# Kernel optimization log

Hardware: AMD Instinct MI355X
Metric: run time of the kernel (lower is better)

The kernel has to match this reference:

```python
import jax, jax.numpy as jnp
import numpy as np

HEADS, OUT_CH = 8, 32  # GATConv(128, 256//8, heads=8) -> concat width 256
NEG_SLOPE = 0.2


def setup_inputs() -> dict:
    key = jax.random.key(0)
    ks = jax.random.split(key, 12)
    N, E, F_IN = 50000, 500000, 128
    H, C = HEADS, OUT_CH
    HID = H * C            # 256
    x = jax.random.normal(ks[0], (N, F_IN), dtype=jnp.float32)
    edge_index = jax.random.randint(ks[1], (2, E), 0, N, dtype=jnp.int64)
    s = 1.0 / np.sqrt(F_IN)
    W_gat = jax.random.normal(ks[2], (F_IN, H * C), dtype=jnp.float32) * s
    att_src = jax.random.normal(ks[3], (H, C), dtype=jnp.float32) * (1.0 / np.sqrt(C))
    att_dst = jax.random.normal(ks[4], (H, C), dtype=jnp.float32) * (1.0 / np.sqrt(C))
    b_gat = jnp.zeros((HID,), dtype=jnp.float32)
    W1 = jax.random.normal(ks[5], (HID, HID // 2), dtype=jnp.float32) * (1.0 / np.sqrt(HID))
    b1 = jnp.zeros((HID // 2,), dtype=jnp.float32)
    W2 = jax.random.normal(ks[6], (HID // 2, 6), dtype=jnp.float32) * (1.0 / np.sqrt(HID // 2))
    b2 = jnp.zeros((6,), dtype=jnp.float32)
    return {"x": x, "edge_index": edge_index, "W_gat": W_gat, "att_src": att_src,
            "att_dst": att_dst, "b_gat": b_gat, "W1": W1, "b1": b1, "W2": W2, "b2": b2}


def _gat_forward(x, edge_index, W_gat, att_src, att_dst, b_gat):
    N = x.shape[0]
    H, C = HEADS, OUT_CH
    # add self loops (PyG GATConv default)
    loop = jnp.arange(N, dtype=edge_index.dtype)
    src = jnp.concatenate([edge_index[0], loop])
    dst = jnp.concatenate([edge_index[1], loop])
    # per-node transform: [N, H, C]
    xh = (x @ W_gat).reshape(N, H, C)
    a_src = jnp.einsum('nhc,hc->nh', xh, att_src)  # [N, H]
    a_dst = jnp.einsum('nhc,hc->nh', xh, att_dst)  # [N, H]
    alpha = a_src[src] + a_dst[dst]                # [Etot, H]
    alpha = jnp.where(alpha >= 0, alpha, NEG_SLOPE * alpha)  # leaky relu
    # segment softmax over destination nodes
    m = jax.ops.segment_max(alpha, dst, num_segments=N)     # [N, H]
    m = jax.lax.stop_gradient(m)
    ex = jnp.exp(alpha - m[dst])
    denom = jax.ops.segment_sum(ex, dst, num_segments=N)    # [N, H]
    coef = ex / denom[dst]                                   # [Etot, H]
    # weighted scatter-add aggregation
    msgs = xh[src] * coef[:, :, None]                        # [Etot, H, C]
    out = jax.ops.segment_sum(msgs, dst, num_segments=N)     # [N, H, C]
    return out.reshape(N, H * C) + b_gat


def reference(x, edge_index, W_gat, att_src, att_dst, b_gat, W1, b1, W2, b2):
    h = _gat_forward(x, edge_index, W_gat, att_src, att_dst, b_gat)
    h = jax.nn.elu(h)
    g = jnp.mean(h, axis=0, keepdims=True)   # [1, 256] mean pool
    g = jax.nn.relu(g @ W1 + b1)
    return g @ W2 + b2                        # [1, 6] logits
```

## Files before the change

kernel.cpp:

```cpp
#include <hip/hip_runtime.h>
#include <hip/hip_fp8.h>
#include <math.h>

#define F_IN 128
#define HID 256
#define NH 8
#define CAP 40

typedef _Float16 h16;
typedef __attribute__((ext_vector_type(8))) _Float16 half8;
typedef __attribute__((ext_vector_type(4))) float f32x4;

__device__ inline unsigned char f32_to_fp8(float v) {
#if __has_builtin(__builtin_amdgcn_cvt_pk_fp8_f32)
    return (unsigned char)(__builtin_amdgcn_cvt_pk_fp8_f32(v, v, 0, false) & 0xff);
#else
    __hip_fp8_e4m3 t(v);
    return (unsigned char)t.__x;
#endif
}

__device__ inline void fp8x4_to_f32(int w, float* out) {
#if __has_builtin(__builtin_amdgcn_cvt_pk_f32_fp8)
    auto lo = __builtin_amdgcn_cvt_pk_f32_fp8(w, false);
    auto hi = __builtin_amdgcn_cvt_pk_f32_fp8(w, true);
    out[0] = lo[0]; out[1] = lo[1]; out[2] = hi[0]; out[3] = hi[1];
#else
    #pragma unroll
    for (int k = 0; k < 4; ++k) {
        __hip_fp8_e4m3 t;
        t.__x = (unsigned char)((w >> (8 * k)) & 0xff);
        out[k] = (float)t;
    }
#endif
}

__global__ void k_prep(const float* __restrict__ Wg, h16* __restrict__ Wt_sw,
                       int* cnt, float* g2, int n) {
    int i = blockIdx.x * 256 + threadIdx.x;
    if (i < n) cnt[i] = 0;
    if (i < 256 * HID) g2[i] = 0.f;
    if (i < 4096) {
        int fid = i;
        int lane16 = fid & 15;
        int quad = (fid >> 4) & 3;
        int ks = (fid >> 6) & 3;
        int ct = fid >> 8;
        int col = ct * 16 + lane16;
        int k0 = ks * 32 + quad * 8;
        half8 v;
        #pragma unroll
        for (int j = 0; j < 8; ++j) v[j] = (h16)Wg[(size_t)(k0 + j) * HID + col];
        *(half8*)(Wt_sw + (size_t)fid * 8) = v;
    }
}

__global__ __launch_bounds__(512) void k_gemmsc(const float* __restrict__ x,
                                                const h16* __restrict__ Wt_sw,
                                                const float* __restrict__ att_s,
                                                const float* __restrict__ att_d,
                                                const int* __restrict__ srcp,
                                                const int* __restrict__ dstp,
                                                unsigned char* __restrict__ xh8,
                                                float* __restrict__ a_src,
                                                float* __restrict__ a_dst,
                                                int* cnt, unsigned short* __restrict__ bin,
                                                int n, int e, int ntiles) {
    __shared__ h16 wlds[32768];
    int t = threadIdx.x;
    {
        const int4* wsrc = (const int4*)Wt_sw;
        int4* wdst = (int4*)wlds;
        #pragma unroll
        for (int i = 0; i < 8; ++i) wdst[i * 512 + t] = wsrc[i * 512 + t];
    }
    __syncthreads();
    int w = t >> 6, l = t & 63;
    int lane16 = l & 15, quad = l >> 4;
    const h16* wl = wlds + (size_t)l * 8;

    auto do_gemm = [&]() {
        for (int tile = blockIdx.x * 8 + w; tile < ntiles; tile += gridDim.x * 8) {
            int row0 = tile * 16;
            int rA = row0 + lane16;
            if (rA >= n) rA = n - 1;
            const float* xrow = x + (size_t)rA * F_IN + quad * 8;
            half8 afr[4];
            #pragma unroll
            for (int ks = 0; ks < 4; ++ks) {
                float4 v0 = *(const float4*)(xrow + ks * 32);
                float4 v1 = *(const float4*)(xrow + ks * 32 + 4);
                half8 a;
                a[0] = (h16)v0.x; a[1] = (h16)v0.y; a[2] = (h16)v0.z; a[3] = (h16)v0.w;
                a[4] = (h16)v1.x; a[5] = (h16)v1.y; a[6] = (h16)v1.z; a[7] = (h16)v1.w;
                afr[ks] = a;
            }
            f32x4 acc[16];
            #pragma unroll
            for (int ct = 0; ct < 16; ++ct) acc[ct] = (f32x4){0.f, 0.f, 0.f, 0.f};
            #pragma unroll
            for (int ct = 0; ct < 16; ++ct) {
                #pragma unroll
                for (int ks = 0; ks < 4; ++ks) {
                    half8 b = *(const half8*)(wl + (ct * 4 + ks) * 512);
                    acc[ct] = __builtin_amdgcn_mfma_f32_16x16x32_f16(afr[ks], b, acc[ct], 0, 0, 0);
                }
            }
            if (row0 + 16 <= n) {
                #pragma unroll
                for (int ct = 0; ct < 16; ++ct) {
                    int col = ct * 16 + lane16;
                    #pragma unroll
                    for (int r = 0; r < 4; ++r)
                        xh8[(size_t)(row0 + quad * 4 + r) * HID + col] = f32_to_fp8(acc[ct][r]);
                }
            } else {
                #pragma unroll
                for (int ct = 0; ct < 16; ++ct) {
                    int col = ct * 16 + lane16;
                    #pragma unroll
                    for (int r = 0; r < 4; ++r) {
                        int row = row0 + quad * 4 + r;
                        if (row < n) xh8[(size_t)row * HID + col] = f32_to_fp8(acc[ct][r]);
                    }
                }
            }
            #pragma unroll
            for (int h = 0; h < 8; ++h) {
                float ps[4] = {0.f, 0.f, 0.f, 0.f};
                float pd[4] = {0.f, 0.f, 0.f, 0.f};
                #pragma unroll
                for (int cc = 0; cc < 2; ++cc) {
                    int ct = h * 2 + cc;
                    float as_ = att_s[ct * 16 + lane16];
                    float ad_ = att_d[ct * 16 + lane16];
                    #pragma unroll
                    for (int r = 0; r < 4; ++r) {
                        ps[r] += acc[ct][r] * as_;
                        pd[r] += acc[ct][r] * ad_;
                    }
                }
                #pragma unroll
                for (int m = 1; m < 16; m <<= 1) {
                    #pragma unroll
                    for (int r = 0; r < 4; ++r) {
                        ps[r] += __shfl_xor(ps[r], m, 64);
                        pd[r] += __shfl_xor(pd[r], m, 64);
                    }
                }
                if (lane16 == 0) {
                    #pragma unroll
                    for (int r = 0; r < 4; ++r) {
                        int row = row0 + quad * 4 + r;
                        if (row < n) {
                            a_src[row * NH + h] = ps[r];
                            a_dst[row * NH + h] = pd[r];
                        }
                    }
                }
            }
        }
    };
    auto do_scatter = [&]() {
        for (int i = blockIdx.x * 512 + t; i < e; i += gridDim.x * 512) {
            int d = dstp[i];
            int pos = atomicAdd(&cnt[d], 1);
            if (pos < CAP) bin[(size_t)d * CAP + pos] = (unsigned short)srcp[i];
        }
    };
    if (blockIdx.x & 1) { do_scatter(); do_gemm(); }
    else                { do_gemm(); do_scatter(); }
}

__global__ __launch_bounds__(256) void k_agg(const unsigned char* __restrict__ xh8,
                                             const float* __restrict__ a_src,
                                             const float* __restrict__ a_dst,
                                             const int* __restrict__ cnt,
                                             const unsigned short* __restrict__ bin,
                                             const float* __restrict__ b_gat,
                                             float* __restrict__ g2, int n) {
    __shared__ float wpart[4][260];
    int t = threadIdx.x;
    int slot = t >> 4;
    int cl = t & 15;
    int c0 = cl * 16;
    int h = cl >> 1;
    int nn = blockIdx.x * 16 + slot;
    bool alive = nn < n;
    int nnc = alive ? nn : (n - 1);

    float ad = a_dst[nnc * NH + h];
    int deg = cnt[nnc];
    if (deg > CAP) deg = CAP;

    float al = a_src[nnc * NH + h] + ad;
    al = al > 0.f ? al : 0.2f * al;
    float ex = __expf(al);
    float den = ex;
    float acc[16];
    {
        int4 v = *(const int4*)(xh8 + (size_t)nnc * HID + c0);
        float f[16];
        fp8x4_to_f32(v.x, f); fp8x4_to_f32(v.y, f + 4);
        fp8x4_to_f32(v.z, f + 8); fp8x4_to_f32(v.w, f + 12);
        #pragma unroll
        for (int i = 0; i < 16; ++i) acc[i] = ex * f[i];
    }
    const unsigned short* brow = bin + (size_t)nnc * CAP;
    int j = 0;
    for (; j + 4 <= deg; j += 4) {
        ushort4 ss = *(const ushort4*)(brow + j);
        int s0 = ss.x, s1 = ss.y, s2 = ss.z, s3 = ss.w;
        float aa[4];
        aa[0] = a_src[s0 * NH + h];
        aa[1] = a_src[s1 * NH + h];
        aa[2] = a_src[s2 * NH + h];
        aa[3] = a_src[s3 * NH + h];
        int4 v0 = *(const int4*)(xh8 + (size_t)s0 * HID + c0);
        int4 v1 = *(const int4*)(xh8 + (size_t)s1 * HID + c0);
        int4 v2 = *(const int4*)(xh8 + (size_t)s2 * HID + c0);
        int4 v3 = *(const int4*)(xh8 + (size_t)s3 * HID + c0);
        float e4[4];
        #pragma unroll
        for (int q = 0; q < 4; ++q) {
            float a2 = aa[q] + ad;
            a2 = a2 > 0.f ? a2 : 0.2f * a2;
            e4[q] = __expf(a2);
            den += e4[q];
        }
        float f[16];
        fp8x4_to_f32(v0.x, f); fp8x4_to_f32(v0.y, f + 4);
        fp8x4_to_f32(v0.z, f + 8); fp8x4_to_f32(v0.w, f + 12);
        #pragma unroll
        for (int i = 0; i < 16; ++i) acc[i] += e4[0] * f[i];
        fp8x4_to_f32(v1.x, f); fp8x4_to_f32(v1.y, f + 4);
        fp8x4_to_f32(v1.z, f + 8); fp8x4_to_f32(v1.w, f + 12);
        #pragma unroll
        for (int i = 0; i < 16; ++i) acc[i] += e4[1] * f[i];
        fp8x4_to_f32(v2.x, f); fp8x4_to_f32(v2.y, f + 4);
        fp8x4_to_f32(v2.z, f + 8); fp8x4_to_f32(v2.w, f + 12);
        #pragma unroll
        for (int i = 0; i < 16; ++i) acc[i] += e4[2] * f[i];
        fp8x4_to_f32(v3.x, f); fp8x4_to_f32(v3.y, f + 4);
        fp8x4_to_f32(v3.z, f + 8); fp8x4_to_f32(v3.w, f + 12);
        #pragma unroll
        for (int i = 0; i < 16; ++i) acc[i] += e4[3] * f[i];
    }
    for (; j < deg; ++j) {
        int s = brow[j];
        float a2 = a_src[s * NH + h] + ad;
        a2 = a2 > 0.f ? a2 : 0.2f * a2;
        float e2 = __expf(a2);
        den += e2;
        int4 v = *(const int4*)(xh8 + (size_t)s * HID + c0);
        float f[16];
        fp8x4_to_f32(v.x, f); fp8x4_to_f32(v.y, f + 4);
        fp8x4_to_f32(v.z, f + 8); fp8x4_to_f32(v.w, f + 12);
        #pragma unroll
        for (int i = 0; i < 16; ++i) acc[i] += e2 * f[i];
    }
    float inv = 1.f / den;
    float val[16];
    #pragma unroll
    for (int q = 0; q < 4; ++q) {
        float4 bv = *(const float4*)(b_gat + c0 + q * 4);
        val[q * 4 + 0] = acc[q * 4 + 0] * inv + bv.x;
        val[q * 4 + 1] = acc[q * 4 + 1] * inv + bv.y;
        val[q * 4 + 2] = acc[q * 4 + 2] * inv + bv.z;
        val[q * 4 + 3] = acc[q * 4 + 3] * inv + bv.w;
    }
    #pragma unroll
    for (int i = 0; i < 16; ++i) {
        float v = val[i];
        v = v > 0.f ? v : expm1f(v);
        val[i] = alive ? v : 0.f;
    }
    #pragma unroll
    for (int i = 0; i < 16; ++i) {
        val[i] += __shfl_xor(val[i], 16, 64);
        val[i] += __shfl_xor(val[i], 32, 64);
    }
    int w = t >> 6, lw = t & 63;
    if (lw < 16) {
        #pragma unroll
        for (int q = 0; q < 4; ++q)
            *(f32x4*)(&wpart[w][c0 + q * 4]) =
                (f32x4){val[q * 4], val[q * 4 + 1], val[q * 4 + 2], val[q * 4 + 3]};
    }
    __syncthreads();
    float s = wpart[0][t] + wpart[1][t] + wpart[2][t] + wpart[3][t];
    atomicAdd(&g2[(blockIdx.x & 255) * HID + t], s);
}

__global__ __launch_bounds__(256) void k_mlp(const float* __restrict__ g2,
                                             const float* __restrict__ W1,
                                             const float* __restrict__ b1,
                                             const float* __restrict__ W2,
                                             const float* __restrict__ b2,
                                             float* __restrict__ out, int n) {
    __shared__ float gm[HID];
    __shared__ float h1p[2][128];
    __shared__ float h1[128];
    int t = threadIdx.x;
    float s = 0.f;
    for (int b = 0; b < 256; ++b) s += g2[b * HID + t];
    gm[t] = s / (float)n;
    __syncthreads();
    int o = t & 127, hf = t >> 7;
    float a = 0.f;
    #pragma unroll 4
    for (int k = hf * 128; k < hf * 128 + 128; ++k) a += gm[k] * W1[k * 128 + o];
    h1p[hf][o] = a;
    __syncthreads();
    if (t < 128) {
        float v = h1p[0][t] + h1p[1][t] + b1[t];
        h1[t] = v > 0.f ? v : 0.f;
    }
    __syncthreads();
    if (t < 6) {
        float a2 = b2[t];
        for (int k = 0; k < 128; ++k) a2 += h1[k] * W2[k * 6 + t];
        out[t] = a2;
    }
}

extern "C" void kernel_launch(void* const* d_in, const int* in_sizes, int n_in,
                              void* d_out, int out_size, void* d_ws, size_t ws_size,
                              hipStream_t stream) {
    const float* x     = (const float*)d_in[0];
    const int*   ei    = (const int*)d_in[1];
    const float* Wg    = (const float*)d_in[2];
    const float* att_s = (const float*)d_in[3];
    const float* att_d = (const float*)d_in[4];
    const float* b_gat = (const float*)d_in[5];
    const float* W1    = (const float*)d_in[6];
    const float* b1    = (const float*)d_in[7];
    const float* W2    = (const float*)d_in[8];
    const float* b2    = (const float*)d_in[9];

    int N = in_sizes[0] / F_IN;
    int E = in_sizes[1] / 2;
    const int* srcp = ei;
    const int* dstp = ei + E;
    int nblk = (N + 15) / 16;
    int ntiles = (N + 15) / 16;

    char* ws = (char*)d_ws;
    size_t off = 0;
    auto alloc = [&](size_t bytes) {
        size_t o = off;
        off += (bytes + 255) & ~(size_t)255;
        return o;
    };
    unsigned char* xh8 = (unsigned char*)(ws + alloc((size_t)N * HID));
    h16*   Wt      = (h16*)(ws + alloc((size_t)F_IN * HID * 2));
    float* asr     = (float*)(ws + alloc((size_t)N * NH * 4));
    float* ads     = (float*)(ws + alloc((size_t)N * NH * 4));
    int*   cnt     = (int*)(ws + alloc((size_t)N * 4));
    unsigned short* bin = (unsigned short*)(ws + alloc((size_t)N * CAP * 2));
    float* g2      = (float*)(ws + alloc((size_t)256 * HID * 4));

    k_prep<<<(N + 255) / 256, 256, 0, stream>>>(Wg, Wt, cnt, g2, N);
    k_gemmsc<<<512, 512, 0, stream>>>(x, Wt, att_s, att_d, srcp, dstp,
                                      xh8, asr, ads, cnt, bin, N, E, ntiles);
    k_agg<<<nblk, 256, 0, stream>>>(xh8, asr, ads, cnt, bin, b_gat, g2, N);
    k_mlp<<<1, 256, 0, stream>>>(g2, W1, b1, W2, b2, (float*)d_out, N);
}
```

Before: 179.6 us.

## Fold attention vectors into GEMM weights and split output columns across block pairs

Precomputes W_gat·att_src and W_gat·att_dst per head as an extra 16-column fp16 weight tile, so a_src/a_dst come from one extra MFMA instead of per-head dot products and shuffle reductions. The GEMM kernel now launches twice as many blocks, with each block pair splitting the 256 output columns in half. This halves LDS use and accumulator registers, which should raise occupancy. The cost is that each x row tile is loaded and converted by both blocks, and the fp16 rounding of the folded weights changes attention-logit precision.

```diff
diff --git a/kernel.cpp b/kernel.cpp
--- a/kernel.cpp
+++ b/kernel.cpp
@@ -35,7 +35,10 @@
 #endif
 }
 
-__global__ void k_prep(const float* __restrict__ Wg, h16* __restrict__ Wt_sw,
+__global__ void k_prep(const float* __restrict__ Wg,
+                       const float* __restrict__ att_s,
+                       const float* __restrict__ att_d,
+                       h16* __restrict__ Wt_sw,
                        int* cnt, float* g2, int n) {
     int i = blockIdx.x * 256 + threadIdx.x;
     if (i < n) cnt[i] = 0;
@@ -53,12 +56,28 @@
         for (int j = 0; j < 8; ++j) v[j] = (h16)Wg[(size_t)(k0 + j) * HID + col];
         *(half8*)(Wt_sw + (size_t)fid * 8) = v;
     }
+    if (i < 256) {
+        int lane16 = i & 15;
+        int quad = (i >> 4) & 3;
+        int ks = i >> 6;
+        int h = lane16 & 7;
+        const float* att = (lane16 < 8) ? att_s : att_d;
+        int k0 = ks * 32 + quad * 8;
+        half8 v;
+        #pragma unroll
+        for (int j = 0; j < 8; ++j) {
+            float s = 0.f;
+            #pragma unroll 8
+            for (int c = 0; c < 32; ++c)
+                s += Wg[(size_t)(k0 + j) * HID + h * 32 + c] * att[h * 32 + c];
+            v[j] = (h16)s;
+        }
+        *(half8*)(Wt_sw + 32768 + (size_t)i * 8) = v;
+    }
 }
 
 __global__ __launch_bounds__(512) void k_gemmsc(const float* __restrict__ x,
                                                 const h16* __restrict__ Wt_sw,
-                                                const float* __restrict__ att_s,
-                                                const float* __restrict__ att_d,
                                                 const int* __restrict__ srcp,
                                                 const int* __restrict__ dstp,
                                                 unsigned char* __restrict__ xh8,
@@ -66,21 +85,29 @@
                                                 float* __restrict__ a_dst,
                                                 int* cnt, unsigned short* __restrict__ bin,
                                                 int n, int e, int ntiles) {
-    __shared__ h16 wlds[32768];
+    __shared__ h16 wlds[18432];
     int t = threadIdx.x;
+    int halfsel = blockIdx.x & 1;
     {
         const int4* wsrc = (const int4*)Wt_sw;
         int4* wdst = (int4*)wlds;
-        #pragma unroll
-        for (int i = 0; i < 8; ++i) wdst[i * 512 + t] = wsrc[i * 512 + t];
+        if (halfsel == 0) {
+            #pragma unroll
+            for (int i = 0; i < 4; ++i) wdst[i * 512 + t] = wsrc[i * 512 + t];
+            if (t < 256) wdst[2048 + t] = wsrc[4096 + t];
+        } else {
+            #pragma unroll
+            for (int i = 0; i < 4; ++i) wdst[i * 512 + t] = wsrc[2048 + i * 512 + t];
+        }
     }
     __syncthreads();
     int w = t >> 6, l = t & 63;
     int lane16 = l & 15, quad = l >> 4;
     const h16* wl = wlds + (size_t)l * 8;
+    int coff = halfsel * 8;
 
     auto do_gemm = [&]() {
-        for (int tile = blockIdx.x * 8 + w; tile < ntiles; tile += gridDim.x * 8) {
+        for (int tile = (blockIdx.x >> 1) * 8 + w; tile < ntiles; tile += (gridDim.x >> 1) * 8) {
             int row0 = tile * 16;
             int rA = row0 + lane16;
             if (rA >= n) rA = n - 1;
@@ -95,11 +122,11 @@
                 a[4] = (h16)v1.x; a[5] = (h16)v1.y; a[6] = (h16)v1.z; a[7] = (h16)v1.w;
                 afr[ks] = a;
             }
-            f32x4 acc[16];
-            #pragma unroll
-            for (int ct = 0; ct < 16; ++ct) acc[ct] = (f32x4){0.f, 0.f, 0.f, 0.f};
-            #pragma unroll
-            for (int ct = 0; ct < 16; ++ct) {
+            f32x4 acc[8];
+            #pragma unroll
+            for (int ct = 0; ct < 8; ++ct) acc[ct] = (f32x4){0.f, 0.f, 0.f, 0.f};
+            #pragma unroll
+            for (int ct = 0; ct < 8; ++ct) {
                 #pragma unroll
                 for (int ks = 0; ks < 4; ++ks) {
                     half8 b = *(const half8*)(wl + (ct * 4 + ks) * 512);
@@ -108,16 +135,16 @@
             }
             if (row0 + 16 <= n) {
                 #pragma unroll
-                for (int ct = 0; ct < 16; ++ct) {
-                    int col = ct * 16 + lane16;
+                for (int ct = 0; ct < 8; ++ct) {
+                    int col = (ct + coff) * 16 + lane16;
                     #pragma unroll
                     for (int r = 0; r < 4; ++r)
                         xh8[(size_t)(row0 + quad * 4 + r) * HID + col] = f32_to_fp8(acc[ct][r]);
                 }
             } else {
                 #pragma unroll
-                for (int ct = 0; ct < 16; ++ct) {
-                    int col = ct * 16 + lane16;
+                for (int ct = 0; ct < 8; ++ct) {
+                    int col = (ct + coff) * 16 + lane16;
                     #pragma unroll
                     for (int r = 0; r < 4; ++r) {
                         int row = row0 + quad * 4 + r;
@@ -125,37 +152,19 @@
                     }
                 }
             }
-            #pragma unroll
-            for (int h = 0; h < 8; ++h) {
-                float ps[4] = {0.f, 0.f, 0.f, 0.f};
-                float pd[4] = {0.f, 0.f, 0.f, 0.f};
-                #pragma unroll
-                for (int cc = 0; cc < 2; ++cc) {
-                    int ct = h * 2 + cc;
-                    float as_ = att_s[ct * 16 + lane16];
-                    float ad_ = att_d[ct * 16 + lane16];
-                    #pragma unroll
-                    for (int r = 0; r < 4; ++r) {
-                        ps[r] += acc[ct][r] * as_;
-                        pd[r] += acc[ct][r] * ad_;
-                    }
-                }
-                #pragma unroll
-                for (int m = 1; m < 16; m <<= 1) {
-                    #pragma unroll
-                    for (int r = 0; r < 4; ++r) {
-                        ps[r] += __shfl_xor(ps[r], m, 64);
-                        pd[r] += __shfl_xor(pd[r], m, 64);
-                    }
-                }
-                if (lane16 == 0) {
-                    #pragma unroll
-                    for (int r = 0; r < 4; ++r) {
-                        int row = row0 + quad * 4 + r;
-                        if (row < n) {
-                            a_src[row * NH + h] = ps[r];
-                            a_dst[row * NH + h] = pd[r];
-                        }
+            if (halfsel == 0) {
+                f32x4 acca = (f32x4){0.f, 0.f, 0.f, 0.f};
+                #pragma unroll
+                for (int ks = 0; ks < 4; ++ks) {
+                    half8 b = *(const half8*)(wl + (32 + ks) * 512);
+                    acca = __builtin_amdgcn_mfma_f32_16x16x32_f16(afr[ks], b, acca, 0, 0, 0);
+                }
+                #pragma unroll
+                for (int r = 0; r < 4; ++r) {
+                    int row = row0 + quad * 4 + r;
+                    if (row < n) {
+                        if (lane16 < 8) a_src[row * NH + lane16] = acca[r];
+                        else            a_dst[row * NH + lane16 - 8] = acca[r];
                     }
                 }
             }
@@ -168,8 +177,8 @@
             if (pos < CAP) bin[(size_t)d * CAP + pos] = (unsigned short)srcp[i];
         }
     };
-    if (blockIdx.x & 1) { do_scatter(); do_gemm(); }
-    else                { do_gemm(); do_scatter(); }
+    if (halfsel) { do_scatter(); do_gemm(); }
+    else         { do_gemm(); do_scatter(); }
 }
 
 __global__ __launch_bounds__(256) void k_agg(const unsigned char* __restrict__ xh8,
@@ -353,16 +362,16 @@
         return o;
     };
     unsigned char* xh8 = (unsigned char*)(ws + alloc((size_t)N * HID));
-    h16*   Wt      = (h16*)(ws + alloc((size_t)F_IN * HID * 2));
+    h16*   Wt      = (h16*)(ws + alloc((size_t)34816 * 2));
     float* asr     = (float*)(ws + alloc((size_t)N * NH * 4));
     float* ads     = (float*)(ws + alloc((size_t)N * NH * 4));
     int*   cnt     = (int*)(ws + alloc((size_t)N * 4));
     unsigned short* bin = (unsigned short*)(ws + alloc((size_t)N * CAP * 2));
     float* g2      = (float*)(ws + alloc((size_t)256 * HID * 4));
 
-    k_prep<<<(N + 255) / 256, 256, 0, stream>>>(Wg, Wt, cnt, g2, N);
-    k_gemmsc<<<512, 512, 0, stream>>>(x, Wt, att_s, att_d, srcp, dstp,
-                                      xh8, asr, ads, cnt, bin, N, E, ntiles);
+    k_prep<<<(N + 255) / 256, 256, 0, stream>>>(Wg, att_s, att_d, Wt, cnt, g2, N);
+    k_gemmsc<<<1024, 512, 0, stream>>>(x, Wt, srcp, dstp,
+                                       xh8, asr, ads, cnt, bin, N, E, ntiles);
     k_agg<<<nblk, 256, 0, stream>>>(xh8, asr, ads, cnt, bin, b_gat, g2, N);
     k_mlp<<<1, 256, 0, stream>>>(g2, W1, b1, W2, b2, (float*)d_out, N);
 }
```

Result: slower. 193.7 us (+7.8%).
